# Kernel optimization log

Hardware: AMD Instinct MI355X
Metric: run time of the kernel (lower is better)

## Reference

```python
import jax, jax.numpy as jnp
import numpy as np

B, NCLS, T, D, L = 32, 20, 2048, 2048, 128
GAMMA = 0.1           # maxGamma temperature
THRES = 0.5           # lcs threshold
FEAT_MARGIN = 50.0
LAMB1, LAMB2, LAMB3 = 1.0, 5e-5, 2e-4
LAMB_LCS, LAMB_FSD = 0.1, 0.1


def _similarity(a, b):
    # row-normalized cosine similarity: [L, d] x [L, d] -> [L, L]
    a = a / jnp.linalg.norm(a, axis=1, keepdims=True)
    b = b / jnp.linalg.norm(b, axis=1, keepdims=True)
    return a @ b.T


def _fsd_dp(m, g):
    # soft-DP: C[i,j] = m[i-1,j-1] + gamma*logsumexp([C[i-1,j-1], g+C[i-1,j], g+C[i,j-1]]/gamma)
    n = m.shape[0]
    def row_step(prev_row, rows):          # prev_row: C[i-1, 0..n]
        m_row, g_row = rows
        def col_step(c_left, xs):
            c_diag, c_up, m_ij, g_ij = xs
            neigh = jnp.stack([c_diag, g_ij + c_up, g_ij + c_left])
            new = m_ij + GAMMA * jax.nn.logsumexp(neigh / GAMMA)
            return new, new
        _, vals = jax.lax.scan(col_step, jnp.zeros((), m.dtype),
                               (prev_row[:-1], prev_row[1:], m_row, g_row))
        new_row = jnp.concatenate([jnp.zeros((1,), m.dtype), vals])
        return new_row, None
    final_row, _ = jax.lax.scan(row_step, jnp.zeros((n + 1,), m.dtype), (m, g))
    return final_row[-1]


def _lcs_dp(s):
    # C[i,j] = C[i-1,j-1]+s if s>thres else max(C[i-1,j], C[i,j-1])
    n = s.shape[0]
    def row_step(prev_row, s_row):
        def col_step(c_left, xs):
            c_diag, c_up, s_ij = xs
            new = jnp.where(s_ij > THRES, c_diag + s_ij, jnp.maximum(c_up, c_left))
            return new, new
        _, vals = jax.lax.scan(col_step, jnp.zeros((), s.dtype),
                               (prev_row[:-1], prev_row[1:], s_row))
        return jnp.concatenate([jnp.zeros((1,), s.dtype), vals]), None
    final_row, _ = jax.lax.scan(row_step, jnp.zeros((n + 1,), s.dtype), s)
    return final_row[-1]


def _fsd_pair(c0, c1):
    h = c0.shape[-1] // 2
    m = _similarity(c0[:, :h], c1[:, :h])
    g = _similarity(c0[:, h:], c1[:, h:])
    return _fsd_dp(m, g)


def _lcs_pair(c0, c1):
    sim = _similarity(c0, c1)
    s = jnp.maximum(0.0, sim - 0.8) * 5.0
    return _lcs_dp(s)


def _cls_criterion(x, lab):
    return -jnp.mean(jnp.sum(jnp.log(x + 1e-45) * lab, axis=1))


def _acm_forward(act_inst_cls, act_cont_cls, act_back_cls, vid_label, temp_att,
                 act_inst_feat, act_cont_feat, act_back_feat, temp_cas,
                 lcs_candi, fsd_act_candi, fsd_bak_candi, pos_pair, neg_pair):
    bsz = act_inst_cls.shape[0]
    zeros = jnp.zeros((bsz, 1), act_inst_cls.dtype)
    ones = jnp.ones((bsz, 1), act_inst_cls.dtype)
    inst_lab = jnp.concatenate([vid_label, zeros], axis=1)
    cont_lab = jnp.concatenate([vid_label, ones], axis=1)
    back_lab = jnp.concatenate([jnp.zeros_like(vid_label), ones], axis=1)
    inst_lab = inst_lab / jnp.sum(inst_lab, axis=1, keepdims=True)
    cont_lab = cont_lab / jnp.sum(cont_lab, axis=1, keepdims=True)
    back_lab = back_lab / jnp.sum(back_lab, axis=1, keepdims=True)
    cls_loss = (_cls_criterion(act_inst_cls, inst_lab)
                + _cls_criterion(act_cont_cls, cont_lab)
                + _cls_criterion(act_back_cls, back_lab))

    guide_loss = jnp.mean(jnp.sum(jnp.abs(
        1.0 - temp_cas[:, :, -1] - jax.lax.stop_gradient(temp_att[:, :, 0])), axis=1))

    n_i = jnp.linalg.norm(act_inst_feat, axis=1)
    n_c = jnp.linalg.norm(act_cont_feat, axis=1)
    n_b = jnp.linalg.norm(act_back_feat, axis=1)
    f1 = jnp.maximum(FEAT_MARGIN - n_i + n_c, 0.0)
    f2 = jnp.maximum(FEAT_MARGIN - n_c + n_b, 0.0)
    feat_loss = jnp.mean((f1 + f2 + n_b) ** 2)

    sparse_loss = jnp.mean(jnp.sum(temp_att[:, :, :2], axis=1))

    acm_loss = cls_loss + LAMB1 * guide_loss + LAMB2 * feat_loss + LAMB3 * sparse_loss

    # LCS branch (pairs are constants)
    pos_lcs = jax.vmap(_lcs_pair)(lcs_candi[pos_pair[:, 0]], lcs_candi[pos_pair[:, 1]]).mean()
    neg_lcs = jax.vmap(_lcs_pair)(lcs_candi[neg_pair[:, 0]], lcs_candi[neg_pair[:, 1]]).mean()
    lcs_loss = neg_lcs - pos_lcs

    # FSD branch
    act_act = jax.vmap(_fsd_pair)(fsd_act_candi[pos_pair[:, 0]], fsd_act_candi[pos_pair[:, 1]]).mean()
    act_bak = jax.vmap(_fsd_pair)(fsd_act_candi[neg_pair[:, 0]], fsd_bak_candi[neg_pair[:, 1]]).mean()
    fsd_loss = act_bak - act_act

    return acm_loss + LAMB_LCS * lcs_loss + LAMB_FSD * fsd_loss


def setup_inputs() -> dict:
    key = jax.random.key(0)
    ks = jax.random.split(key, 12)
    # single-label videos: 16 classes, each appearing twice -> 16 pos pairs
    classes = np.arange(B) % 16
    vid_label = jnp.asarray(np.eye(NCLS, dtype=np.float32)[classes])
    pos_pair = jnp.asarray(np.stack([np.arange(16), np.arange(16) + 16], axis=1).astype(np.int32))
    neg_pair = jnp.asarray(np.stack([np.arange(16), np.arange(16) + 1], axis=1).astype(np.int32))
    return {
        "act_inst_cls": jax.random.uniform(ks[0], (B, NCLS + 1), jnp.float32),
        "act_cont_cls": jax.random.uniform(ks[1], (B, NCLS + 1), jnp.float32),
        "act_back_cls": jax.random.uniform(ks[2], (B, NCLS + 1), jnp.float32),
        "vid_label": vid_label,
        "temp_att": jax.random.uniform(ks[3], (B, T, 3), jnp.float32),
        "act_inst_feat": jax.random.normal(ks[4], (B, D), jnp.float32),
        "act_cont_feat": jax.random.normal(ks[5], (B, D), jnp.float32),
        "act_back_feat": jax.random.normal(ks[6], (B, D), jnp.float32),
        "temp_cas": jax.random.uniform(ks[7], (B, T, NCLS + 1), jnp.float32),
        "lcs_candi": jax.random.normal(ks[8], (B, L, D), jnp.float32),
        "fsd_act_candi": jax.random.normal(ks[9], (B, L, D), jnp.float32),
        "fsd_bak_candi": jax.random.normal(ks[10], (B, L, D), jnp.float32),
        "pos_pair": pos_pair,
        "neg_pair": neg_pair,
    }


def reference(act_inst_cls, act_cont_cls, act_back_cls, vid_label, temp_att,
              act_inst_feat, act_cont_feat, act_back_feat, temp_cas,
              lcs_candi, fsd_act_candi, fsd_bak_candi, pos_pair, neg_pair):
    return _acm_forward(act_inst_cls, act_cont_cls, act_back_cls, vid_label, temp_att,
                        act_inst_feat, act_cont_feat, act_back_feat, temp_cas,
                        lcs_candi, fsd_act_candi, fsd_bak_candi, pos_pair, neg_pair)
```

## Files before the change

### kernel.cpp

```cpp
#include <hip/hip_runtime.h>
#include <hip/hip_bf16.h>
#include <math.h>

#define B_    32
#define NCLS_ 20
#define T_    2048
#define D_    2048
#define L_    128
#define NPAIR 16

#define OFF_SIM_LCS  0
#define OFF_SIM_M    524288
#define OFF_SIM_G    1048576
#define OFF_RN       1572864
#define OFF_NFEAT    1593344
#define OFF_LCS_RES  1593440
#define OFF_FSD_RES  1593472
#define OFF_ACC      1593504

typedef __attribute__((ext_vector_type(8))) short bf16x8;
typedef __attribute__((ext_vector_type(4))) float f32x4;

__device__ __forceinline__ ushort f2bf(float f) {
    __hip_bfloat16 h = __float2bfloat16(f);
    return *reinterpret_cast<ushort*>(&h);
}

__global__ __launch_bounds__(64) void norm_all_kernel(
        const float* __restrict__ lcs, const float* __restrict__ fa,
        const float* __restrict__ fb, const float* __restrict__ fi,
        const float* __restrict__ fc, const float* __restrict__ fbk,
        float* __restrict__ ws) {
    int b = blockIdx.x;
    const float* src; float* dst; int len4; int recip = 1;
    float* rn = ws + OFF_RN;
    if (b < 4096) {
        src = lcs + (size_t)b * 2048; dst = rn + b; len4 = 512;
    } else if (b < 20480) {
        int region = (b - 4096) >> 12;
        int r = (b - 4096) & 4095;
        const float* base = (region < 2) ? fa : fb;
        src = base + (size_t)r * 2048 + (region & 1) * 1024;
        dst = rn + b; len4 = 256;
    } else {
        int r = b - 20480;
        const float* base = (r < 32) ? fi : (r < 64 ? fc : fbk);
        src = base + (size_t)(r & 31) * 2048;
        dst = ws + OFF_NFEAT + r; len4 = 512; recip = 0;
    }
    const float4* p = (const float4*)src;
    float s = 0.f;
    for (int i = threadIdx.x; i < len4; i += 64) {
        float4 v = p[i];
        s += v.x * v.x + v.y * v.y + v.z * v.z + v.w * v.w;
    }
    #pragma unroll
    for (int off = 32; off; off >>= 1) s += __shfl_down(s, off);
    if (threadIdx.x == 0) *dst = recip ? rsqrtf(s) : sqrtf(s);
}

__global__ __launch_bounds__(256) void sim_mfma_kernel(
        const float* __restrict__ lcs, const float* __restrict__ fa,
        const float* __restrict__ fb, const int* __restrict__ pos,
        const int* __restrict__ neg, float* __restrict__ ws) {
    const float* rn = ws + OFF_RN;
    int job = blockIdx.x;

    const float *Aptr, *Bptr, *rnA, *rnB;
    float* out;
    int K, mode;

    if (job < 32) {
        int pi = job & 15;
        const int* pp = (job >= 16) ? neg : pos;
        int p0 = pp[2 * pi], p1 = pp[2 * pi + 1];
        Aptr = lcs + (size_t)p0 * L_ * D_;
        Bptr = lcs + (size_t)p1 * L_ * D_;
        rnA = rn + p0 * L_;
        rnB = rn + p1 * L_;
        out = ws + OFF_SIM_LCS + (size_t)job * L_ * L_;
        K = 2048; mode = 0;
    } else {
        int idx = job - 32;
        int isneg = idx >= 32;
        int ll = idx & 31;
        int pi = ll >> 1, half = ll & 1;
        const int* pp = isneg ? neg : pos;
        int p0 = pp[2 * pi], p1 = pp[2 * pi + 1];
        const float* Bbase = isneg ? fb : fa;
        Aptr = fa + (size_t)p0 * L_ * D_ + half * 1024;
        Bptr = Bbase + (size_t)p1 * L_ * D_ + half * 1024;
        rnA = rn + 4096 + half * 4096 + p0 * L_;
        rnB = rn + 4096 + (isneg ? 8192 : 0) + half * 4096 + p1 * L_;
        int slot = (isneg ? 16 : 0) + pi;
        out = ws + (half ? OFF_SIM_G : OFF_SIM_M) + (size_t)slot * L_ * L_;
        K = 1024; mode = 1;
    }

    __shared__ ushort lA[128 * 64];
    __shared__ ushort lB[128 * 64];
    int tid = threadIdx.x;
    int lane = tid & 63;
    int w = tid >> 6;
    int wr = w >> 1, wc = w & 1;
    int lrow = lane & 15, lhk = lane >> 4;

    f32x4 acc[4][4];
    #pragma unroll
    for (int m = 0; m < 4; ++m)
        #pragma unroll
        for (int n = 0; n < 4; ++n)
            acc[m][n] = (f32x4){0.f, 0.f, 0.f, 0.f};

    for (int k0 = 0; k0 < K; k0 += 64) {
        __syncthreads();
        #pragma unroll
        for (int i = 0; i < 4; ++i) {
            int c = tid + i * 256;
            int row = c >> 3, kb = c & 7;
            int idx = ((row * 64 + kb * 8) ^ ((row & 7) << 3));
            const float* sA = Aptr + (size_t)row * D_ + k0 + kb * 8;
            float4 a0 = *(const float4*)sA;
            float4 a1 = *(const float4*)(sA + 4);
            bf16x8 sv;
            sv[0] = (short)f2bf(a0.x); sv[1] = (short)f2bf(a0.y);
            sv[2] = (short)f2bf(a0.z); sv[3] = (short)f2bf(a0.w);
            sv[4] = (short)f2bf(a1.x); sv[5] = (short)f2bf(a1.y);
            sv[6] = (short)f2bf(a1.z); sv[7] = (short)f2bf(a1.w);
            *(bf16x8*)&lA[idx] = sv;
            const float* sB = Bptr + (size_t)row * D_ + k0 + kb * 8;
            float4 b0 = *(const float4*)sB;
            float4 b1 = *(const float4*)(sB + 4);
            bf16x8 sw;
            sw[0] = (short)f2bf(b0.x); sw[1] = (short)f2bf(b0.y);
            sw[2] = (short)f2bf(b0.z); sw[3] = (short)f2bf(b0.w);
            sw[4] = (short)f2bf(b1.x); sw[5] = (short)f2bf(b1.y);
            sw[6] = (short)f2bf(b1.z); sw[7] = (short)f2bf(b1.w);
            *(bf16x8*)&lB[idx] = sw;
        }
        __syncthreads();
        #pragma unroll
        for (int ks = 0; ks < 2; ++ks) {
            int kbase = ks * 32 + lhk * 8;
            bf16x8 afr[4], bfr[4];
            #pragma unroll
            for (int m = 0; m < 4; ++m) {
                int row = wr * 64 + m * 16 + lrow;
                int idx = ((row * 64 + kbase) ^ ((row & 7) << 3));
                afr[m] = *(const bf16x8*)&lA[idx];
            }
            #pragma unroll
            for (int n = 0; n < 4; ++n) {
                int row = wc * 64 + n * 16 + lrow;
                int idx = ((row * 64 + kbase) ^ ((row & 7) << 3));
                bfr[n] = *(const bf16x8*)&lB[idx];
            }
            #pragma unroll
            for (int m = 0; m < 4; ++m)
                #pragma unroll
                for (int n = 0; n < 4; ++n)
                    acc[m][n] = __builtin_amdgcn_mfma_f32_16x16x32_bf16(
                        afr[m], bfr[n], acc[m][n], 0, 0, 0);
        }
    }

    #pragma unroll
    for (int m = 0; m < 4; ++m) {
        #pragma unroll
        for (int n = 0; n < 4; ++n) {
            int jj = wc * 64 + n * 16 + lrow;
            float rbv = rnB[jj];
            #pragma unroll
            for (int r = 0; r < 4; ++r) {
                int ii = wr * 64 + m * 16 + lhk * 4 + r;
                float v = acc[m][n][r] * rnA[ii] * rbv;
                if (mode == 0) v = fmaxf((v - 0.8f) * 5.0f, 0.f);
                out[ii * L_ + jj] = v;
            }
        }
    }
}

__global__ __launch_bounds__(64) void lcs_dp_kernel(const float* __restrict__ ws_simlcs,
                                                    float* __restrict__ res) {
    int job = blockIdx.x;
    const float* S = ws_simlcs + (size_t)job * L_ * L_;
    int l = threadIdx.x;
    int ra = 2 * l, rb = 2 * l + 1;
    const float* Sa = S + ra * L_;
    const float* Sb = S + rb * L_;
    float a = 0.f, a_prev = 0.f, b = 0.f, u_prev = 0.f;
    float sa_buf[8], sb_buf[8];
    #pragma unroll
    for (int p = 0; p < 8; ++p) {
        sa_buf[p] = Sa[min(max(p - ra, 0), 127)];
        sb_buf[p] = Sb[min(max(p - rb, 0), 127)];
    }
    #pragma unroll 8
    for (int t = 0; t < 256; ++t) {
        int slot = t & 7;
        float sa = sa_buf[slot], sb = sb_buf[slot];
        int ja = t - ra, jb = t - rb;
        float u = __shfl_up(b, 1);
        if (l == 0) u = 0.f;
        float newa = (sa > 0.5f) ? (u_prev + sa) : fmaxf(u, a);
        float newb = (sb > 0.5f) ? (a_prev + sb) : fmaxf(a, b);
        a_prev = a;
        if (ja >= 0 && ja < 128) a = newa;
        if (jb >= 0 && jb < 128) b = newb;
        u_prev = u;
        sa_buf[slot] = Sa[min(max(t + 8 - ra, 0), 127)];
        sb_buf[slot] = Sb[min(max(t + 8 - rb, 0), 127)];
    }
    if (l == 63) res[job] = b;
}

__global__ __launch_bounds__(64) void fsd_dp_kernel(const float* __restrict__ wsm,
                                                    const float* __restrict__ wsg,
                                                    float* __restrict__ res) {
    int job = blockIdx.x;
    const float* M = wsm + (size_t)job * L_ * L_;
    const float* G = wsg + (size_t)job * L_ * L_;
    int l = threadIdx.x;
    int ra = 2 * l, rb = 2 * l + 1;
    const float* Ma = M + ra * L_; const float* Mb = M + rb * L_;
    const float* Ga = G + ra * L_; const float* Gb = G + rb * L_;
    float a = 0.f, a_prev = 0.f, b = 0.f, u_prev = 0.f;
    float mab[8], gab[8], mbb[8], gbb[8];
    #pragma unroll
    for (int p = 0; p < 8; ++p) {
        int ja = min(max(p - ra, 0), 127), jb = min(max(p - rb, 0), 127);
        mab[p] = Ma[ja]; gab[p] = Ga[ja];
        mbb[p] = Mb[jb]; gbb[p] = Gb[jb];
    }
    #pragma unroll 8
    for (int t = 0; t < 256; ++t) {
        int slot = t & 7;
        float ma = mab[slot], ga = gab[slot], mb = mbb[slot], gb = gbb[slot];
        int ja = t - ra, jb = t - rb;
        float u = __shfl_up(b, 1);
        if (l == 0) u = 0.f;
        float x0 = u_prev, x1 = ga + u, x2 = ga + a;
        float mx = fmaxf(x0, fmaxf(x1, x2));
        float e0 = __expf((x0 - mx) * 10.f);
        float e1 = __expf((x1 - mx) * 10.f);
        float e2 = __expf((x2 - mx) * 10.f);
        float newa = ma + mx + 0.1f * __logf(e0 + e1 + e2);
        float y0 = a_prev, y1 = gb + a, y2 = gb + b;
        float my = fmaxf(y0, fmaxf(y1, y2));
        float f0 = __expf((y0 - my) * 10.f);
        float f1 = __expf((y1 - my) * 10.f);
        float f2 = __expf((y2 - my) * 10.f);
        float newb = mb + my + 0.1f * __logf(f0 + f1 + f2);
        a_prev = a;
        if (ja >= 0 && ja < 128) a = newa;
        if (jb >= 0 && jb < 128) b = newb;
        u_prev = u;
        int jan = min(max(t + 8 - ra, 0), 127), jbn = min(max(t + 8 - rb, 0), 127);
        mab[slot] = Ma[jan]; gab[slot] = Ga[jan];
        mbb[slot] = Mb[jbn]; gbb[slot] = Gb[jbn];
    }
    if (l == 63) res[job] = b;
}

__global__ __launch_bounds__(256) void guide_sparse_kernel(const float* __restrict__ temp_att,
                                                           const float* __restrict__ temp_cas,
                                                           float* __restrict__ acc) {
    float g = 0.f, sp = 0.f;
    int n = B_ * T_;
    for (int idx = blockIdx.x * blockDim.x + threadIdx.x; idx < n;
         idx += gridDim.x * blockDim.x) {
        float cas = temp_cas[(size_t)idx * (NCLS_ + 1) + NCLS_];
        float a0 = temp_att[(size_t)idx * 3 + 0];
        float a1 = temp_att[(size_t)idx * 3 + 1];
        g += fabsf(1.f - cas - a0);
        sp += a0 + a1;
    }
    #pragma unroll
    for (int off = 32; off; off >>= 1) {
        g += __shfl_down(g, off);
        sp += __shfl_down(sp, off);
    }
    if ((threadIdx.x & 63) == 0) {
        atomicAdd(&acc[0], g);
        atomicAdd(&acc[1], sp);
    }
}

__global__ __launch_bounds__(64) void final_kernel(const float* __restrict__ xi,
                                                   const float* __restrict__ xc,
                                                   const float* __restrict__ xb,
                                                   const float* __restrict__ vl,
                                                   const float* __restrict__ ws,
                                                   float* __restrict__ out) {
    const float* nfeat = ws + OFF_NFEAT;
    const float* lcs_res = ws + OFF_LCS_RES;
    const float* fsd_res = ws + OFF_FSD_RES;
    const float* acc = ws + OFF_ACC;
    int lane = threadIdx.x;
    float part = 0.f;

    if (lane < B_) {
        int b = lane;
        float sv = 0.f;
        for (int j = 0; j < NCLS_; ++j) sv += vl[b * NCLS_ + j];
        float inv_i = 1.f / sv;
        float inv_c = 1.f / (sv + 1.f);
        float si = 0.f, sc = 0.f;
        for (int j = 0; j < NCLS_; ++j) {
            float lab = vl[b * NCLS_ + j];
            if (lab != 0.f) {
                si += logf(xi[b * (NCLS_ + 1) + j] + 1e-45f) * lab * inv_i;
                sc += logf(xc[b * (NCLS_ + 1) + j] + 1e-45f) * lab * inv_c;
            }
        }
        sc += logf(xc[b * (NCLS_ + 1) + NCLS_] + 1e-45f) * inv_c;
        float sb = logf(xb[b * (NCLS_ + 1) + NCLS_] + 1e-45f);
        float cls = -(si + sc + sb) / (float)B_;

        float ni = nfeat[b], nc = nfeat[B_ + b], nb = nfeat[2 * B_ + b];
        float f1 = fmaxf(50.f - ni + nc, 0.f);
        float f2 = fmaxf(50.f - nc + nb, 0.f);
        float fv = f1 + f2 + nb;
        float feat = fv * fv / (float)B_;

        float sgn = (b < NPAIR) ? -1.f : 1.f;
        float lcs = sgn * lcs_res[b] / (float)NPAIR;
        float fsd = sgn * fsd_res[b] / (float)NPAIR;

        part = cls + 5e-5f * feat + 0.1f * (lcs + fsd);
    }
    #pragma unroll
    for (int off = 32; off; off >>= 1) part += __shfl_down(part, off);
    if (lane == 0) {
        float guide = acc[0] / (float)B_;
        float sparse = acc[1] / (float)B_;
        out[0] = part + guide + 2e-4f * sparse;
    }
}

extern "C" void kernel_launch(void* const* d_in, const int* in_sizes, int n_in,
                              void* d_out, int out_size, void* d_ws, size_t ws_size,
                              hipStream_t stream) {
    const float* act_inst_cls = (const float*)d_in[0];
    const float* act_cont_cls = (const float*)d_in[1];
    const float* act_back_cls = (const float*)d_in[2];
    const float* vid_label    = (const float*)d_in[3];
    const float* temp_att     = (const float*)d_in[4];
    const float* act_inst_feat= (const float*)d_in[5];
    const float* act_cont_feat= (const float*)d_in[6];
    const float* act_back_feat= (const float*)d_in[7];
    const float* temp_cas     = (const float*)d_in[8];
    const float* lcs_candi    = (const float*)d_in[9];
    const float* fsd_act      = (const float*)d_in[10];
    const float* fsd_bak      = (const float*)d_in[11];
    const int*   pos_pair     = (const int*)d_in[12];
    const int*   neg_pair     = (const int*)d_in[13];

    float* ws = (float*)d_ws;
    float* out = (float*)d_out;

    hipMemsetAsync(ws + OFF_ACC, 0, 2 * sizeof(float), stream);

    hipLaunchKernelGGL(norm_all_kernel, dim3(20576), dim3(64), 0, stream,
                       lcs_candi, fsd_act, fsd_bak,
                       act_inst_feat, act_cont_feat, act_back_feat, ws);

    hipLaunchKernelGGL(sim_mfma_kernel, dim3(96), dim3(256), 0, stream,
                       lcs_candi, fsd_act, fsd_bak, pos_pair, neg_pair, ws);

    hipLaunchKernelGGL(lcs_dp_kernel, dim3(32), dim3(64), 0, stream,
                       ws + OFF_SIM_LCS, ws + OFF_LCS_RES);
    hipLaunchKernelGGL(fsd_dp_kernel, dim3(32), dim3(64), 0, stream,
                       ws + OFF_SIM_M, ws + OFF_SIM_G, ws + OFF_FSD_RES);

    hipLaunchKernelGGL(guide_sparse_kernel, dim3(64), dim3(256), 0, stream,
                       temp_att, temp_cas, ws + OFF_ACC);

    hipLaunchKernelGGL(final_kernel, dim3(1), dim3(64), 0, stream,
                       act_inst_cls, act_cont_cls, act_back_cls, vid_label,
                       ws, out);
}
```

Measured before the change: 314.5 us.

## Split-K similarity GEMM with double buffering, fused DP kernel, tiled guide loss

The similarity GEMM is split along K into 4 (LCS) or 2 (FSD) slices, which raises the grid from 96 to 256 blocks, and it double-buffers the LDS tiles with register prefetch. Partial sums go to the workspace. A merged DP kernel reduces the partials, applies the norm scaling and LCS transform, stages the matrices in shared memory, and runs both DP recurrences from LDS. The guide/sparse kernel now stages contiguous tiles through shared memory over a larger grid, and the GEMM is launched before the norm kernel. In exchange, the partial outputs add extra workspace traffic and the DP kernel uses 128KB of shared memory per block.

```diff
diff --git a/kernel.cpp b/kernel.cpp
--- a/kernel.cpp
+++ b/kernel.cpp
@@ -9,14 +9,15 @@
 #define L_    128
 #define NPAIR 16
 
-#define OFF_SIM_LCS  0
-#define OFF_SIM_M    524288
-#define OFF_SIM_G    1048576
-#define OFF_RN       1572864
-#define OFF_NFEAT    1593344
-#define OFF_LCS_RES  1593440
-#define OFF_FSD_RES  1593472
-#define OFF_ACC      1593504
+#define OFF_LCS_PART 0
+#define OFF_M_PART   2097152
+#define OFF_G_PART   3145728
+#define OFF_RN       4194304
+#define OFF_NFEAT    4214784
+#define OFF_LCS_RES  4214880
+#define OFF_FSD_RES  4214912
+#define OFF_ACC      4214944
+#define SLICE_STRIDE 524288
 
 typedef __attribute__((ext_vector_type(8))) short bf16x8;
 typedef __attribute__((ext_vector_type(4))) float f32x4;
@@ -63,48 +64,50 @@
         const float* __restrict__ lcs, const float* __restrict__ fa,
         const float* __restrict__ fb, const int* __restrict__ pos,
         const int* __restrict__ neg, float* __restrict__ ws) {
-    const float* rn = ws + OFF_RN;
-    int job = blockIdx.x;
-
-    const float *Aptr, *Bptr, *rnA, *rnB;
+    int bid = blockIdx.x;
+    const float *Aptr, *Bptr;
     float* out;
-    int K, mode;
-
-    if (job < 32) {
+
+    if (bid < 128) {
+        int job = bid >> 2, ks = bid & 3;
         int pi = job & 15;
         const int* pp = (job >= 16) ? neg : pos;
         int p0 = pp[2 * pi], p1 = pp[2 * pi + 1];
-        Aptr = lcs + (size_t)p0 * L_ * D_;
-        Bptr = lcs + (size_t)p1 * L_ * D_;
-        rnA = rn + p0 * L_;
-        rnB = rn + p1 * L_;
-        out = ws + OFF_SIM_LCS + (size_t)job * L_ * L_;
-        K = 2048; mode = 0;
+        Aptr = lcs + (size_t)p0 * L_ * D_ + ks * 512;
+        Bptr = lcs + (size_t)p1 * L_ * D_ + ks * 512;
+        out = ws + OFF_LCS_PART + ((size_t)ks * 32 + job) * 16384;
     } else {
-        int idx = job - 32;
-        int isneg = idx >= 32;
-        int ll = idx & 31;
-        int pi = ll >> 1, half = ll & 1;
+        int e = bid - 128;
+        int fj = e >> 1, ks = e & 1;
+        int isneg = fj >= 32;
+        int q = fj & 31;
+        int pi = q >> 1, half = q & 1;
         const int* pp = isneg ? neg : pos;
         int p0 = pp[2 * pi], p1 = pp[2 * pi + 1];
         const float* Bbase = isneg ? fb : fa;
-        Aptr = fa + (size_t)p0 * L_ * D_ + half * 1024;
-        Bptr = Bbase + (size_t)p1 * L_ * D_ + half * 1024;
-        rnA = rn + 4096 + half * 4096 + p0 * L_;
-        rnB = rn + 4096 + (isneg ? 8192 : 0) + half * 4096 + p1 * L_;
+        Aptr = fa + (size_t)p0 * L_ * D_ + half * 1024 + ks * 512;
+        Bptr = Bbase + (size_t)p1 * L_ * D_ + half * 1024 + ks * 512;
         int slot = (isneg ? 16 : 0) + pi;
-        out = ws + (half ? OFF_SIM_G : OFF_SIM_M) + (size_t)slot * L_ * L_;
-        K = 1024; mode = 1;
-    }
-
-    __shared__ ushort lA[128 * 64];
-    __shared__ ushort lB[128 * 64];
+        out = ws + (half ? OFF_G_PART : OFF_M_PART) + ((size_t)ks * 32 + slot) * 16384;
+    }
+
+    __shared__ ushort lA[2][128 * 64];
+    __shared__ ushort lB[2][128 * 64];
     int tid = threadIdx.x;
     int lane = tid & 63;
     int w = tid >> 6;
     int wr = w >> 1, wc = w & 1;
     int lrow = lane & 15, lhk = lane >> 4;
 
+    int srow[4], skb[4];
+    #pragma unroll
+    for (int i = 0; i < 4; ++i) {
+        int c = tid + i * 256;
+        srow[i] = c >> 3; skb[i] = c & 7;
+    }
+
+    float4 pa0[4], pa1[4], pb0[4], pb1[4];
+
     f32x4 acc[4][4];
     #pragma unroll
     for (int m = 0; m < 4; ++m)
@@ -112,33 +115,42 @@
         for (int n = 0; n < 4; ++n)
             acc[m][n] = (f32x4){0.f, 0.f, 0.f, 0.f};
 
-    for (int k0 = 0; k0 < K; k0 += 64) {
-        __syncthreads();
-        #pragma unroll
-        for (int i = 0; i < 4; ++i) {
-            int c = tid + i * 256;
-            int row = c >> 3, kb = c & 7;
-            int idx = ((row * 64 + kb * 8) ^ ((row & 7) << 3));
-            const float* sA = Aptr + (size_t)row * D_ + k0 + kb * 8;
-            float4 a0 = *(const float4*)sA;
-            float4 a1 = *(const float4*)(sA + 4);
-            bf16x8 sv;
-            sv[0] = (short)f2bf(a0.x); sv[1] = (short)f2bf(a0.y);
-            sv[2] = (short)f2bf(a0.z); sv[3] = (short)f2bf(a0.w);
-            sv[4] = (short)f2bf(a1.x); sv[5] = (short)f2bf(a1.y);
-            sv[6] = (short)f2bf(a1.z); sv[7] = (short)f2bf(a1.w);
-            *(bf16x8*)&lA[idx] = sv;
-            const float* sB = Bptr + (size_t)row * D_ + k0 + kb * 8;
-            float4 b0 = *(const float4*)sB;
-            float4 b1 = *(const float4*)(sB + 4);
-            bf16x8 sw;
-            sw[0] = (short)f2bf(b0.x); sw[1] = (short)f2bf(b0.y);
-            sw[2] = (short)f2bf(b0.z); sw[3] = (short)f2bf(b0.w);
-            sw[4] = (short)f2bf(b1.x); sw[5] = (short)f2bf(b1.y);
-            sw[6] = (short)f2bf(b1.z); sw[7] = (short)f2bf(b1.w);
-            *(bf16x8*)&lB[idx] = sw;
-        }
-        __syncthreads();
+    #pragma unroll
+    for (int i = 0; i < 4; ++i) {
+        const float* sA = Aptr + (size_t)srow[i] * D_ + skb[i] * 8;
+        pa0[i] = *(const float4*)sA; pa1[i] = *(const float4*)(sA + 4);
+        const float* sB = Bptr + (size_t)srow[i] * D_ + skb[i] * 8;
+        pb0[i] = *(const float4*)sB; pb1[i] = *(const float4*)(sB + 4);
+    }
+    #pragma unroll
+    for (int i = 0; i < 4; ++i) {
+        int idx = ((srow[i] * 64 + skb[i] * 8) ^ ((srow[i] & 7) << 3));
+        bf16x8 sv, sw;
+        sv[0] = (short)f2bf(pa0[i].x); sv[1] = (short)f2bf(pa0[i].y);
+        sv[2] = (short)f2bf(pa0[i].z); sv[3] = (short)f2bf(pa0[i].w);
+        sv[4] = (short)f2bf(pa1[i].x); sv[5] = (short)f2bf(pa1[i].y);
+        sv[6] = (short)f2bf(pa1[i].z); sv[7] = (short)f2bf(pa1[i].w);
+        *(bf16x8*)&lA[0][idx] = sv;
+        sw[0] = (short)f2bf(pb0[i].x); sw[1] = (short)f2bf(pb0[i].y);
+        sw[2] = (short)f2bf(pb0[i].z); sw[3] = (short)f2bf(pb0[i].w);
+        sw[4] = (short)f2bf(pb1[i].x); sw[5] = (short)f2bf(pb1[i].y);
+        sw[6] = (short)f2bf(pb1[i].z); sw[7] = (short)f2bf(pb1[i].w);
+        *(bf16x8*)&lB[0][idx] = sw;
+    }
+    __syncthreads();
+
+    #pragma unroll
+    for (int t = 0; t < 8; ++t) {
+        if (t < 7) {
+            int k0 = (t + 1) * 64;
+            #pragma unroll
+            for (int i = 0; i < 4; ++i) {
+                const float* sA = Aptr + (size_t)srow[i] * D_ + k0 + skb[i] * 8;
+                pa0[i] = *(const float4*)sA; pa1[i] = *(const float4*)(sA + 4);
+                const float* sB = Bptr + (size_t)srow[i] * D_ + k0 + skb[i] * 8;
+                pb0[i] = *(const float4*)sB; pb1[i] = *(const float4*)(sB + 4);
+            }
+        }
         #pragma unroll
         for (int ks = 0; ks < 2; ++ks) {
             int kbase = ks * 32 + lhk * 8;
@@ -147,13 +159,13 @@
             for (int m = 0; m < 4; ++m) {
                 int row = wr * 64 + m * 16 + lrow;
                 int idx = ((row * 64 + kbase) ^ ((row & 7) << 3));
-                afr[m] = *(const bf16x8*)&lA[idx];
+                afr[m] = *(const bf16x8*)&lA[t & 1][idx];
             }
             #pragma unroll
             for (int n = 0; n < 4; ++n) {
                 int row = wc * 64 + n * 16 + lrow;
                 int idx = ((row * 64 + kbase) ^ ((row & 7) << 3));
-                bfr[n] = *(const bf16x8*)&lB[idx];
+                bfr[n] = *(const bf16x8*)&lB[t & 1][idx];
             }
             #pragma unroll
             for (int m = 0; m < 4; ++m)
@@ -162,6 +174,24 @@
                     acc[m][n] = __builtin_amdgcn_mfma_f32_16x16x32_bf16(
                         afr[m], bfr[n], acc[m][n], 0, 0, 0);
         }
+        if (t < 7) {
+            #pragma unroll
+            for (int i = 0; i < 4; ++i) {
+                int idx = ((srow[i] * 64 + skb[i] * 8) ^ ((srow[i] & 7) << 3));
+                bf16x8 sv, sw;
+                sv[0] = (short)f2bf(pa0[i].x); sv[1] = (short)f2bf(pa0[i].y);
+                sv[2] = (short)f2bf(pa0[i].z); sv[3] = (short)f2bf(pa0[i].w);
+                sv[4] = (short)f2bf(pa1[i].x); sv[5] = (short)f2bf(pa1[i].y);
+                sv[6] = (short)f2bf(pa1[i].z); sv[7] = (short)f2bf(pa1[i].w);
+                *(bf16x8*)&lA[(t + 1) & 1][idx] = sv;
+                sw[0] = (short)f2bf(pb0[i].x); sw[1] = (short)f2bf(pb0[i].y);
+                sw[2] = (short)f2bf(pb0[i].z); sw[3] = (short)f2bf(pb0[i].w);
+                sw[4] = (short)f2bf(pb1[i].x); sw[5] = (short)f2bf(pb1[i].y);
+                sw[6] = (short)f2bf(pb1[i].z); sw[7] = (short)f2bf(pb1[i].w);
+                *(bf16x8*)&lB[(t + 1) & 1][idx] = sw;
+            }
+        }
+        __syncthreads();
     }
 
     #pragma unroll
@@ -169,119 +199,176 @@
         #pragma unroll
         for (int n = 0; n < 4; ++n) {
             int jj = wc * 64 + n * 16 + lrow;
-            float rbv = rnB[jj];
             #pragma unroll
             for (int r = 0; r < 4; ++r) {
                 int ii = wr * 64 + m * 16 + lhk * 4 + r;
-                float v = acc[m][n][r] * rnA[ii] * rbv;
-                if (mode == 0) v = fmaxf((v - 0.8f) * 5.0f, 0.f);
-                out[ii * L_ + jj] = v;
-            }
-        }
-    }
-}
-
-__global__ __launch_bounds__(64) void lcs_dp_kernel(const float* __restrict__ ws_simlcs,
-                                                    float* __restrict__ res) {
+                out[ii * L_ + jj] = acc[m][n][r];
+            }
+        }
+    }
+}
+
+__global__ __launch_bounds__(64) void dp_kernel(const int* __restrict__ pos,
+                                                const int* __restrict__ neg,
+                                                float* __restrict__ ws) {
+    __shared__ float Sm[128 * 128];
+    __shared__ float Sg[128 * 128];
     int job = blockIdx.x;
-    const float* S = ws_simlcs + (size_t)job * L_ * L_;
-    int l = threadIdx.x;
-    int ra = 2 * l, rb = 2 * l + 1;
-    const float* Sa = S + ra * L_;
-    const float* Sb = S + rb * L_;
+    int lane = threadIdx.x;
+    const float* rn = ws + OFF_RN;
+    bool is_lcs = job < 32;
+
+    if (is_lcs) {
+        int pi = job & 15;
+        const int* pp = (job >= 16) ? neg : pos;
+        int p0 = pp[2 * pi], p1 = pp[2 * pi + 1];
+        const float* P = ws + OFF_LCS_PART + (size_t)job * 16384;
+        const float* rA = rn + p0 * 128;
+        const float* rB = rn + p1 * 128;
+        for (int c = 0; c < 64; ++c) {
+            int base = (c * 64 + lane) * 4;
+            int r = base >> 7, j0 = base & 127;
+            float4 v0 = *(const float4*)&P[base];
+            float4 v1 = *(const float4*)&P[SLICE_STRIDE + base];
+            float4 v2 = *(const float4*)&P[2 * SLICE_STRIDE + base];
+            float4 v3 = *(const float4*)&P[3 * SLICE_STRIDE + base];
+            float ra = rA[r];
+            float4 rb = *(const float4*)&rB[j0];
+            float4 sv;
+            sv.x = fmaxf(((v0.x + v1.x + v2.x + v3.x) * ra * rb.x - 0.8f) * 5.f, 0.f);
+            sv.y = fmaxf(((v0.y + v1.y + v2.y + v3.y) * ra * rb.y - 0.8f) * 5.f, 0.f);
+            sv.z = fmaxf(((v0.z + v1.z + v2.z + v3.z) * ra * rb.z - 0.8f) * 5.f, 0.f);
+            sv.w = fmaxf(((v0.w + v1.w + v2.w + v3.w) * ra * rb.w - 0.8f) * 5.f, 0.f);
+            *(float4*)&Sm[base] = sv;
+        }
+    } else {
+        int fj = job - 32;
+        int isneg = fj >= 16;
+        int pi = fj & 15;
+        const int* pp = isneg ? neg : pos;
+        int p0 = pp[2 * pi], p1 = pp[2 * pi + 1];
+        const float* Pm = ws + OFF_M_PART + (size_t)fj * 16384;
+        const float* Pg = ws + OFF_G_PART + (size_t)fj * 16384;
+        const float* rAm = rn + 4096 + p0 * 128;
+        const float* rBm = rn + (isneg ? 12288 : 4096) + p1 * 128;
+        const float* rAg = rn + 8192 + p0 * 128;
+        const float* rBg = rn + (isneg ? 16384 : 8192) + p1 * 128;
+        for (int c = 0; c < 64; ++c) {
+            int base = (c * 64 + lane) * 4;
+            int r = base >> 7, j0 = base & 127;
+            float4 m0 = *(const float4*)&Pm[base];
+            float4 m1 = *(const float4*)&Pm[SLICE_STRIDE + base];
+            float4 g0 = *(const float4*)&Pg[base];
+            float4 g1 = *(const float4*)&Pg[SLICE_STRIDE + base];
+            float ram = rAm[r], rag = rAg[r];
+            float4 rbm = *(const float4*)&rBm[j0];
+            float4 rbg = *(const float4*)&rBg[j0];
+            float4 mv, gv;
+            mv.x = (m0.x + m1.x) * ram * rbm.x;
+            mv.y = (m0.y + m1.y) * ram * rbm.y;
+            mv.z = (m0.z + m1.z) * ram * rbm.z;
+            mv.w = (m0.w + m1.w) * ram * rbm.w;
+            gv.x = (g0.x + g1.x) * rag * rbg.x;
+            gv.y = (g0.y + g1.y) * rag * rbg.y;
+            gv.z = (g0.z + g1.z) * rag * rbg.z;
+            gv.w = (g0.w + g1.w) * rag * rbg.w;
+            *(float4*)&Sm[base] = mv;
+            *(float4*)&Sg[base] = gv;
+        }
+    }
+    __syncthreads();
+
+    int ra = 2 * lane, rb = 2 * lane + 1;
     float a = 0.f, a_prev = 0.f, b = 0.f, u_prev = 0.f;
-    float sa_buf[8], sb_buf[8];
-    #pragma unroll
-    for (int p = 0; p < 8; ++p) {
-        sa_buf[p] = Sa[min(max(p - ra, 0), 127)];
-        sb_buf[p] = Sb[min(max(p - rb, 0), 127)];
-    }
-    #pragma unroll 8
-    for (int t = 0; t < 256; ++t) {
-        int slot = t & 7;
-        float sa = sa_buf[slot], sb = sb_buf[slot];
-        int ja = t - ra, jb = t - rb;
-        float u = __shfl_up(b, 1);
-        if (l == 0) u = 0.f;
-        float newa = (sa > 0.5f) ? (u_prev + sa) : fmaxf(u, a);
-        float newb = (sb > 0.5f) ? (a_prev + sb) : fmaxf(a, b);
-        a_prev = a;
-        if (ja >= 0 && ja < 128) a = newa;
-        if (jb >= 0 && jb < 128) b = newb;
-        u_prev = u;
-        sa_buf[slot] = Sa[min(max(t + 8 - ra, 0), 127)];
-        sb_buf[slot] = Sb[min(max(t + 8 - rb, 0), 127)];
-    }
-    if (l == 63) res[job] = b;
-}
-
-__global__ __launch_bounds__(64) void fsd_dp_kernel(const float* __restrict__ wsm,
-                                                    const float* __restrict__ wsg,
-                                                    float* __restrict__ res) {
-    int job = blockIdx.x;
-    const float* M = wsm + (size_t)job * L_ * L_;
-    const float* G = wsg + (size_t)job * L_ * L_;
-    int l = threadIdx.x;
-    int ra = 2 * l, rb = 2 * l + 1;
-    const float* Ma = M + ra * L_; const float* Mb = M + rb * L_;
-    const float* Ga = G + ra * L_; const float* Gb = G + rb * L_;
-    float a = 0.f, a_prev = 0.f, b = 0.f, u_prev = 0.f;
-    float mab[8], gab[8], mbb[8], gbb[8];
-    #pragma unroll
-    for (int p = 0; p < 8; ++p) {
-        int ja = min(max(p - ra, 0), 127), jb = min(max(p - rb, 0), 127);
-        mab[p] = Ma[ja]; gab[p] = Ga[ja];
-        mbb[p] = Mb[jb]; gbb[p] = Gb[jb];
-    }
-    #pragma unroll 8
-    for (int t = 0; t < 256; ++t) {
-        int slot = t & 7;
-        float ma = mab[slot], ga = gab[slot], mb = mbb[slot], gb = gbb[slot];
-        int ja = t - ra, jb = t - rb;
-        float u = __shfl_up(b, 1);
-        if (l == 0) u = 0.f;
-        float x0 = u_prev, x1 = ga + u, x2 = ga + a;
-        float mx = fmaxf(x0, fmaxf(x1, x2));
-        float e0 = __expf((x0 - mx) * 10.f);
-        float e1 = __expf((x1 - mx) * 10.f);
-        float e2 = __expf((x2 - mx) * 10.f);
-        float newa = ma + mx + 0.1f * __logf(e0 + e1 + e2);
-        float y0 = a_prev, y1 = gb + a, y2 = gb + b;
-        float my = fmaxf(y0, fmaxf(y1, y2));
-        float f0 = __expf((y0 - my) * 10.f);
-        float f1 = __expf((y1 - my) * 10.f);
-        float f2 = __expf((y2 - my) * 10.f);
-        float newb = mb + my + 0.1f * __logf(f0 + f1 + f2);
-        a_prev = a;
-        if (ja >= 0 && ja < 128) a = newa;
-        if (jb >= 0 && jb < 128) b = newb;
-        u_prev = u;
-        int jan = min(max(t + 8 - ra, 0), 127), jbn = min(max(t + 8 - rb, 0), 127);
-        mab[slot] = Ma[jan]; gab[slot] = Ga[jan];
-        mbb[slot] = Mb[jbn]; gbb[slot] = Gb[jbn];
-    }
-    if (l == 63) res[job] = b;
-}
-
-__global__ __launch_bounds__(256) void guide_sparse_kernel(const float* __restrict__ temp_att,
-                                                           const float* __restrict__ temp_cas,
+
+    if (is_lcs) {
+        const float* Sa = Sm + ra * 128;
+        const float* Sb = Sm + rb * 128;
+        float sa_buf[4], sb_buf[4];
+        #pragma unroll
+        for (int p = 0; p < 4; ++p) {
+            sa_buf[p] = Sa[min(max(p - ra, 0), 127)];
+            sb_buf[p] = Sb[min(max(p - rb, 0), 127)];
+        }
+        #pragma unroll 4
+        for (int t = 0; t < 256; ++t) {
+            int slot = t & 3;
+            float sa = sa_buf[slot], sb = sb_buf[slot];
+            int ja = t - ra, jb = t - rb;
+            float u = __shfl_up(b, 1);
+            if (lane == 0) u = 0.f;
+            float newa = (sa > 0.5f) ? (u_prev + sa) : fmaxf(u, a);
+            float newb = (sb > 0.5f) ? (a_prev + sb) : fmaxf(a, b);
+            a_prev = a;
+            if (ja >= 0 && ja < 128) a = newa;
+            if (jb >= 0 && jb < 128) b = newb;
+            u_prev = u;
+            sa_buf[slot] = Sa[min(max(t + 4 - ra, 0), 127)];
+            sb_buf[slot] = Sb[min(max(t + 4 - rb, 0), 127)];
+        }
+        if (lane == 63) ws[OFF_LCS_RES + job] = b;
+    } else {
+        const float* Ma = Sm + ra * 128; const float* Mb = Sm + rb * 128;
+        const float* Ga = Sg + ra * 128; const float* Gb = Sg + rb * 128;
+        float mab[4], gab[4], mbb[4], gbb[4];
+        #pragma unroll
+        for (int p = 0; p < 4; ++p) {
+            int ja = min(max(p - ra, 0), 127), jb = min(max(p - rb, 0), 127);
+            mab[p] = Ma[ja]; gab[p] = Ga[ja];
+            mbb[p] = Mb[jb]; gbb[p] = Gb[jb];
+        }
+        #pragma unroll 4
+        for (int t = 0; t < 256; ++t) {
+            int slot = t & 3;
+            float ma = mab[slot], ga = gab[slot], mb = mbb[slot], gb = gbb[slot];
+            int ja = t - ra, jb = t - rb;
+            float u = __shfl_up(b, 1);
+            if (lane == 0) u = 0.f;
+            float x0 = u_prev, x1 = ga + u, x2 = ga + a;
+            float mx = fmaxf(x0, fmaxf(x1, x2));
+            float e0 = __expf((x0 - mx) * 10.f);
+            float e1 = __expf((x1 - mx) * 10.f);
+            float e2 = __expf((x2 - mx) * 10.f);
+            float newa = ma + mx + 0.1f * __logf(e0 + e1 + e2);
+            float y0 = a_prev, y1 = gb + a, y2 = gb + b;
+            float my = fmaxf(y0, fmaxf(y1, y2));
+            float f0 = __expf((y0 - my) * 10.f);
+            float f1 = __expf((y1 - my) * 10.f);
+            float f2 = __expf((y2 - my) * 10.f);
+            float newb = mb + my + 0.1f * __logf(f0 + f1 + f2);
+            a_prev = a;
+            if (ja >= 0 && ja < 128) a = newa;
+            if (jb >= 0 && jb < 128) b = newb;
+            u_prev = u;
+            int jan = min(max(t + 4 - ra, 0), 127), jbn = min(max(t + 4 - rb, 0), 127);
+            mab[slot] = Ma[jan]; gab[slot] = Ga[jan];
+            mbb[slot] = Mb[jbn]; gbb[slot] = Gb[jbn];
+        }
+        if (lane == 63) ws[OFF_FSD_RES + (job - 32)] = b;
+    }
+}
+
+__global__ __launch_bounds__(256) void guide_sparse_kernel(const float* __restrict__ att,
+                                                           const float* __restrict__ cas,
                                                            float* __restrict__ acc) {
-    float g = 0.f, sp = 0.f;
-    int n = B_ * T_;
-    for (int idx = blockIdx.x * blockDim.x + threadIdx.x; idx < n;
-         idx += gridDim.x * blockDim.x) {
-        float cas = temp_cas[(size_t)idx * (NCLS_ + 1) + NCLS_];
-        float a0 = temp_att[(size_t)idx * 3 + 0];
-        float a1 = temp_att[(size_t)idx * 3 + 1];
-        g += fabsf(1.f - cas - a0);
-        sp += a0 + a1;
-    }
+    __shared__ float sc[256 * 21];
+    __shared__ float sa[256 * 3];
+    int tid = threadIdx.x;
+    size_t b0 = (size_t)blockIdx.x * 256;
+    const float4* pc = (const float4*)(cas + b0 * 21);
+    for (int i = tid; i < 1344; i += 256) *(float4*)&sc[i * 4] = pc[i];
+    const float4* pa = (const float4*)(att + b0 * 3);
+    for (int i = tid; i < 192; i += 256) *(float4*)&sa[i * 4] = pa[i];
+    __syncthreads();
+    float a0 = sa[tid * 3], a1 = sa[tid * 3 + 1];
+    float g = fabsf(1.f - sc[tid * 21 + 20] - a0);
+    float sp = a0 + a1;
     #pragma unroll
     for (int off = 32; off; off >>= 1) {
         g += __shfl_down(g, off);
         sp += __shfl_down(sp, off);
     }
-    if ((threadIdx.x & 63) == 0) {
+    if ((tid & 63) == 0) {
         atomicAdd(&acc[0], g);
         atomicAdd(&acc[1], sp);
     }
@@ -362,20 +449,18 @@
 
     hipMemsetAsync(ws + OFF_ACC, 0, 2 * sizeof(float), stream);
 
+    hipLaunchKernelGGL(sim_mfma_kernel, dim3(256), dim3(256), 0, stream,
+                       lcs_candi, fsd_act, fsd_bak, pos_pair, neg_pair, ws);
+
     hipLaunchKernelGGL(norm_all_kernel, dim3(20576), dim3(64), 0, stream,
                        lcs_candi, fsd_act, fsd_bak,
                        act_inst_feat, act_cont_feat, act_back_feat, ws);
 
-    hipLaunchKernelGGL(sim_mfma_kernel, dim3(96), dim3(256), 0, stream,
-                       lcs_candi, fsd_act, fsd_bak, pos_pair, neg_pair, ws);
-
-    hipLaunchKernelGGL(lcs_dp_kernel, dim3(32), dim3(64), 0, stream,
-                       ws + OFF_SIM_LCS, ws + OFF_LCS_RES);
-    hipLaunchKernelGGL(fsd_dp_kernel, dim3(32), dim3(64), 0, stream,
-                       ws + OFF_SIM_M, ws + OFF_SIM_G, ws + OFF_FSD_RES);
-
-    hipLaunchKernelGGL(guide_sparse_kernel, dim3(64), dim3(256), 0, stream,
+    hipLaunchKernelGGL(guide_sparse_kernel, dim3(256), dim3(256), 0, stream,
                        temp_att, temp_cas, ws + OFF_ACC);
+
+    hipLaunchKernelGGL(dp_kernel, dim3(64), dim3(64), 0, stream,
+                       pos_pair, neg_pair, ws);
 
     hipLaunchKernelGGL(final_kernel, dim3(1), dim3(64), 0, stream,
                        act_inst_cls, act_cont_cls, act_back_cls, vid_label,
```

After: 279.9 us. 1.12x faster.
